# Kernel optimization log

Measured on AMD Instinct MI355X. Metric: run time of the kernel, lower is better.

## Reference

```python
import jax, jax.numpy as jnp
import numpy as np


def setup_inputs() -> dict:
    key = jax.random.key(0)
    ks = jax.random.split(key, 8)
    B, C, W, H = 4, 256, 64, 64
    Cq = C // 8
    return {
        "input": jax.random.normal(ks[0], (B, C, W, H), dtype=jnp.float32),
        "Wf": jax.random.normal(ks[1], (Cq, C), dtype=jnp.float32) * 0.05,
        "bf": jax.random.normal(ks[2], (Cq,), dtype=jnp.float32) * 0.05,
        "Wg": jax.random.normal(ks[3], (Cq, C), dtype=jnp.float32) * 0.05,
        "bg": jax.random.normal(ks[4], (Cq,), dtype=jnp.float32) * 0.05,
        "Wh": jax.random.normal(ks[5], (C, C), dtype=jnp.float32) * 0.05,
        "bh": jax.random.normal(ks[6], (C,), dtype=jnp.float32) * 0.05,
        "gamma": jax.random.normal(ks[7], (1,), dtype=jnp.float32),
    }


def reference(input, Wf, bf, Wg, bg, Wh, bh, gamma):
    # input: [B, C, W, H]; SAGAN self-attention over N = W*H spatial tokens.
    B, C, W, H = input.shape
    N = W * H
    x = input.reshape(B, C, N)
    # 1x1 Conv1d == per-token linear projection over channels.
    f = jnp.einsum('oc,bcn->bon', Wf, x) + bf[None, :, None]  # [B, C/8, N]
    g = jnp.einsum('oc,bcn->bon', Wg, x) + bg[None, :, None]  # [B, C/8, N]
    h = jnp.einsum('oc,bcn->bon', Wh, x) + bh[None, :, None]  # [B, C,   N]
    # s = f^T g -> [B, N, N]; softmax over last dim (columns / g-tokens).
    s = jnp.einsum('bon,bom->bnm', f, g)
    attention = jax.nn.softmax(s, axis=-1)
    # out = h @ attention^T : out[b,c,m] = sum_n h[b,c,n] * attention[b,m,n]
    out = jnp.einsum('bcn,bmn->bcm', h, attention)
    out = out.reshape(B, C, W, H)
    return gamma[0] * out + input
```

## Files before the change

### kernel.cpp

```cpp
#include <hip/hip_runtime.h>

typedef _Float16 half8 __attribute__((ext_vector_type(8)));
typedef _Float16 half4 __attribute__((ext_vector_type(4)));
typedef __fp16 f16x2 __attribute__((ext_vector_type(2)));
typedef __fp16 f16x4 __attribute__((ext_vector_type(4)));
typedef float floatx16 __attribute__((ext_vector_type(16)));

#define MFMA_F16(A, B, C) __builtin_amdgcn_mfma_f32_32x32x16_f16(A, B, C, 0, 0, 0)

constexpr int Bn = 4;
constexpr int Cc = 256;
constexpr int Cq = 32;
constexpr int Nn = 4096;
constexpr float LOG2E = 1.44269504088896340736f;


__device__ inline floatx16 zero16() {
  floatx16 z;
#pragma unroll
  for (int i = 0; i < 16; ++i) z[i] = 0.f;
  return z;
}

__global__ __launch_bounds__(256) void k_wconv(
    const float* __restrict__ Wf, const float* __restrict__ Wg,
    const float* __restrict__ Wh, _Float16* __restrict__ Wfh,
    _Float16* __restrict__ Wgh, _Float16* __restrict__ Whh) {
  int e = (blockIdx.x * 256 + threadIdx.x) * 4;
  const float* src;
  _Float16* dst;
  float sc = 1.f;
  if (e < 8192) { src = Wf + e; dst = Wfh + e; sc = LOG2E; }
  else if (e < 16384) { src = Wg + (e - 8192); dst = Wgh + (e - 8192); }
  else { src = Wh + (e - 16384); dst = Whh + (e - 16384); }
  float4 v = *(const float4*)src;
  half4 o;
  o[0] = (_Float16)(v.x * sc); o[1] = (_Float16)(v.y * sc);
  o[2] = (_Float16)(v.z * sc); o[3] = (_Float16)(v.w * sc);
  *(half4*)dst = o;
}

__global__ __launch_bounds__(256) void k_proj(
    const float* __restrict__ x,
    const _Float16* __restrict__ Wfh, const float* __restrict__ bf,
    const _Float16* __restrict__ Wgh, const float* __restrict__ bg,
    const _Float16* __restrict__ Whh, const float* __restrict__ bh,
    _Float16* __restrict__ Q, _Float16* __restrict__ K4,
    _Float16* __restrict__ V8) {
  __shared__ float xs[32][260];
  int tid = threadIdx.x;
  int w = tid >> 6, lane = tid & 63;
  int ml = lane & 31, h = lane >> 5;
  int b = blockIdx.x >> 7, nt = blockIdx.x & 127;
  int n0 = nt * 32;

  {
    int c = tid >> 3;
    int nl = (tid & 7) * 4;
    const float* xp = x + (size_t)b * Cc * Nn + n0 + nl;
#pragma unroll
    for (int pass = 0; pass < 8; ++pass) {
      int cc = c + pass * 32;
      float4 v = *(const float4*)(xp + (size_t)cc * Nn);
      xs[nl + 0][cc] = v.x;
      xs[nl + 1][cc] = v.y;
      xs[nl + 2][cc] = v.z;
      xs[nl + 3][cc] = v.w;
    }
  }
  __syncthreads();

  half8 bfr[16];
#pragma unroll
  for (int kc = 0; kc < 16; ++kc) {
    const float* xp = &xs[ml][kc * 16 + h * 8];
    half8 f;
#pragma unroll
    for (int j = 0; j < 8; ++j) f[j] = (_Float16)xp[j];
    bfr[kc] = f;
  }

  for (int t = w; t < 10; t += 4) {
    const _Float16* W;
    const float* bias;
    float bscale = 1.f;
    int o0 = 0;
    if (t == 0) { W = Wfh; bias = bf; bscale = LOG2E; }
    else if (t == 1) { W = Wgh; bias = bg; }
    else { W = Whh + (size_t)(t - 2) * 32 * Cc; bias = bh + (t - 2) * 32; o0 = (t - 2) * 32; }

    floatx16 acc = zero16();
    const _Float16* wp = W + (size_t)ml * Cc + h * 8;
#pragma unroll
    for (int kc = 0; kc < 16; ++kc) {
      half8 a = *(const half8*)(wp + kc * 16);
      acc = MFMA_F16(a, bfr[kc], acc);
    }

    if (t == 0) {
      _Float16* op = Q + ((size_t)b * Nn + n0 + ml) * Cq;
#pragma unroll
      for (int qd = 0; qd < 4; ++qd) {
        float4 bq = *(const float4*)(bias + 8 * qd + 4 * h);
        const float* bqp = (const float*)&bq;
#pragma unroll
        for (int i = 0; i < 4; ++i) {
          int crow = i + 8 * qd + 4 * h;
          op[crow] = (_Float16)(acc[4 * qd + i] + bqp[i] * bscale);
        }
      }
    } else if (t == 1) {
#pragma unroll
      for (int qd = 0; qd < 4; ++qd) {
        float4 bq = *(const float4*)(bias + 8 * qd + 4 * h);
        const float* bqp = (const float*)&bq;
#pragma unroll
        for (int i = 0; i < 4; ++i) {
          int crow = i + 8 * qd + 4 * h;
          K4[(((size_t)b * 4 + (crow >> 3)) * Nn + n0 + ml) * 8 + (crow & 7)] =
              (_Float16)(acc[4 * qd + i] + bqp[i]);
        }
      }
    } else {
      size_t nb = (size_t)((n0 + ml) >> 3);
      _Float16* op = V8 + (((size_t)b * 512 + nb) * 256) * 8 + (ml & 7);
#pragma unroll
      for (int qd = 0; qd < 4; ++qd) {
        float4 bq = *(const float4*)(bias + 8 * qd + 4 * h);
        const float* bqp = (const float*)&bq;
#pragma unroll
        for (int i = 0; i < 4; ++i) {
          int crow = i + 8 * qd + 4 * h;
          op[(size_t)(o0 + crow) * 8] = (_Float16)(acc[4 * qd + i] + bqp[i]);
        }
      }
    }
  }
}

__global__ __launch_bounds__(512) void k_rowmax(const _Float16* __restrict__ Q,
                                                const _Float16* __restrict__ K4,
                                                float* __restrict__ M) {
  __shared__ float red[8][32];
  int tid = threadIdx.x, w = tid >> 6, lane = tid & 63;
  int ml = lane & 31, h = lane >> 5;
  int b = blockIdx.x >> 7, mt = blockIdx.x & 127;
  int m0 = mt * 32;
  const _Float16* qp = Q + ((size_t)b * Nn + m0 + ml) * Cq + h * 8;
  half8 qb0 = *(const half8*)(qp);
  half8 qb1 = *(const half8*)(qp + 16);
  const _Float16* kp0 = K4 + (((size_t)b * 4 + h) * Nn + w * 512 + ml) * 8;
  const _Float16* kp1 = K4 + (((size_t)b * 4 + 2 + h) * Nn + w * 512 + ml) * 8;
  float mx = -3.0e38f;
  for (int t = 0; t < 16; ++t) {
    floatx16 s = zero16();
    half8 k0 = *(const half8*)(kp0 + (size_t)t * 32 * 8);
    half8 k1 = *(const half8*)(kp1 + (size_t)t * 32 * 8);
    s = MFMA_F16(k0, qb0, s);
    s = MFMA_F16(k1, qb1, s);
#pragma unroll
    for (int i = 0; i < 16; ++i) mx = fmaxf(mx, s[i]);
  }
  mx = fmaxf(mx, __shfl_xor(mx, 32, 64));
  if (h == 0) red[w][ml] = mx;
  __syncthreads();
  if (tid < 32) {
    float m2 = red[0][tid];
#pragma unroll
    for (int i = 1; i < 8; ++i) m2 = fmaxf(m2, red[i][tid]);
    M[(size_t)b * Nn + m0 + tid] = m2;
  }
}

__global__ __launch_bounds__(512, 4) void k_attn(
    const _Float16* __restrict__ Q, const _Float16* __restrict__ K4,
    const _Float16* __restrict__ V8, const float* __restrict__ M,
    _Float16* __restrict__ Opart, float* __restrict__ lpart, int nspan) {
  __shared__ _Float16 P[2 * 64 * 128];
  __shared__ float lred[8][32];
  int tid = threadIdx.x, w = tid >> 6, lane = tid & 63;
  int ml = lane & 31, h = lane >> 5;
  int msub = w & 1, nq = w >> 1;
  int bx = blockIdx.x;
  int mt = bx & 63, b = (bx >> 6) & 3, nc = bx >> 8;
  int m0 = mt * 64;
  int nbase0 = nc * nspan;
  int sw = ml & 15;

  const _Float16* qp = Q + ((size_t)b * Nn + m0 + msub * 32 + ml) * Cq + h * 8;
  half8 qb0 = *(const half8*)(qp);
  half8 qb1 = *(const half8*)(qp + 16);
  float Mv = M[(size_t)b * Nn + m0 + msub * 32 + ml];
  float lacc = 0.f;

  const _Float16* k4b0 =
      K4 + (((size_t)b * 4 + h) * Nn + nbase0 + nq * 32 + ml) * 8;
  const _Float16* k4b1 =
      K4 + (((size_t)b * 4 + 2 + h) * Nn + nbase0 + nq * 32 + ml) * 8;

  int c0 = w * 32;
  const _Float16* v8b =
      V8 + (((size_t)b * 512 + (nbase0 >> 3)) * 256 + c0 + ml) * 8;

  floatx16 o0 = zero16(), o1 = zero16();
  int iters = nspan >> 7;
  _Float16* pwbase = &P[(msub * 32 + ml) * 128];
  const _Float16* pr0 = &P[ml * 128];
  const _Float16* pr1 = &P[(32 + ml) * 128];

  for (int it = 0; it < iters; ++it) {
    int bufo = (it & 1) * (64 * 128);
    {
      floatx16 s = zero16();
      half8 k0 = *(const half8*)(k4b0 + (size_t)it * 128 * 8);
      half8 k1 = *(const half8*)(k4b1 + (size_t)it * 128 * 8);
      s = MFMA_F16(k0, qb0, s);
      s = MFMA_F16(k1, qb1, s);
      _Float16* pw = pwbase + bufo;
#pragma unroll
      for (int q = 0; q < 4; ++q) {
        float p0 = __builtin_amdgcn_exp2f(s[4 * q + 0] - Mv);
        float p1 = __builtin_amdgcn_exp2f(s[4 * q + 1] - Mv);
        float p2 = __builtin_amdgcn_exp2f(s[4 * q + 2] - Mv);
        float p3 = __builtin_amdgcn_exp2f(s[4 * q + 3] - Mv);
        lacc += (p0 + p1) + (p2 + p3);
        f16x4 pkv = __builtin_shufflevector(__builtin_amdgcn_cvt_pkrtz(p0, p1),
                                            __builtin_amdgcn_cvt_pkrtz(p2, p3),
                                            0, 1, 2, 3);
        half4 pk = __builtin_bit_cast(half4, pkv);
        *(half4*)(pw + ((nq * 4 + q) ^ sw) * 8 + 4 * h) = pk;
      }
    }
    __syncthreads();
    {
      const _Float16* vp = v8b + (size_t)it * 16 * 2048;
      const _Float16* p0b = pr0 + bufo;
      const _Float16* p1b = pr1 + bufo;
#pragma unroll
      for (int kc = 0; kc < 8; ++kc) {
        half8 vf = *(const half8*)(vp + (size_t)(kc * 2 + h) * 2048);
        int chunk = (kc * 2 + h) ^ sw;
        half8 pb0 = *(const half8*)(p0b + chunk * 8);
        half8 pb1 = *(const half8*)(p1b + chunk * 8);
        o0 = MFMA_F16(vf, pb0, o0);
        o1 = MFMA_F16(vf, pb1, o1);
      }
    }
  }

  lacc += __shfl_xor(lacc, 32, 64);
  if (h == 0) lred[w][ml] = lacc;
  __syncthreads();
  if (w < 2 && h == 0) {
    float lsum = lred[w][ml] + lred[w + 2][ml] + lred[w + 4][ml] + lred[w + 6][ml];
    lpart[((size_t)nc * Bn + b) * Nn + m0 + w * 32 + ml] = lsum;
  }

  _Float16* op0 = Opart + ((size_t)((size_t)nc * Bn + b) * Cc) * Nn + (m0 + ml);
#pragma unroll
  for (int r = 0; r < 16; ++r) {
    int c = c0 + (r & 3) + 8 * (r >> 2) + 4 * h;
    op0[(size_t)c * Nn] = (_Float16)o0[r];
    op0[(size_t)c * Nn + 32] = (_Float16)o1[r];
  }
}

__global__ __launch_bounds__(256) void k_fin(const _Float16* __restrict__ Op,
                                             const float* __restrict__ lp,
                                             const float* __restrict__ inp,
                                             const float* __restrict__ gamma,
                                             float* __restrict__ out, int NC) {
  int i4 = (blockIdx.x * 256 + threadIdx.x) * 4;
  int m = i4 & (Nn - 1);
  int bc = i4 >> 12;
  int b = bc >> 8;
  float ax = 0.f, ay = 0.f, az = 0.f, aw = 0.f;
  float lx = 0.f, ly = 0.f, lz = 0.f, lw = 0.f;
  for (int nc = 0; nc < NC; ++nc) {
    half4 o = *(const half4*)(Op + ((size_t)nc * Bn * Cc + bc) * Nn + m);
    float4 lv = *(const float4*)(lp + ((size_t)nc * Bn + b) * Nn + m);
    ax += (float)o[0]; ay += (float)o[1]; az += (float)o[2]; aw += (float)o[3];
    lx += lv.x; ly += lv.y; lz += lv.z; lw += lv.w;
  }
  float g = gamma[0];
  float4 xi = *(const float4*)(inp + (size_t)i4);
  float4 r;
  r.x = g * ax / lx + xi.x;
  r.y = g * ay / ly + xi.y;
  r.z = g * az / lz + xi.z;
  r.w = g * aw / lw + xi.w;
  *(float4*)(out + (size_t)i4) = r;
}

extern "C" void kernel_launch(void* const* d_in, const int* in_sizes, int n_in,
                              void* d_out, int out_size, void* d_ws,
                              size_t ws_size, hipStream_t stream) {
  const float* x = (const float*)d_in[0];
  const float* Wf = (const float*)d_in[1];
  const float* bf = (const float*)d_in[2];
  const float* Wg = (const float*)d_in[3];
  const float* bg = (const float*)d_in[4];
  const float* Wh = (const float*)d_in[5];
  const float* bh = (const float*)d_in[6];
  const float* gamma = (const float*)d_in[7];
  float* out = (float*)d_out;

  char* ws = (char*)d_ws;
  _Float16* Q  = (_Float16*)(ws);
  _Float16* K4 = (_Float16*)(ws + 1048576);
  _Float16* V8 = (_Float16*)(ws + 2097152);
  float*    M  = (float*)   (ws + 10485760);
  _Float16* Wfh = (_Float16*)(ws + 10551296);
  _Float16* Wgh = (_Float16*)(ws + 10567680);
  _Float16* Whh = (_Float16*)(ws + 10584064);

  size_t base = 10715136u;
  size_t per_chunk = 65536u + 8388608u;
  int NC = (ws_size >= base + 2u * per_chunk) ? 2 : 1;
  int nspan = Nn / NC;

  float*    lpart = (float*)(ws + base);
  _Float16* Opart = (_Float16*)(ws + base + (size_t)NC * 65536u);

  k_wconv<<<dim3(80), dim3(256), 0, stream>>>(Wf, Wg, Wh, Wfh, Wgh, Whh);
  k_proj<<<dim3(512), dim3(256), 0, stream>>>(x, Wfh, bf, Wgh, bg, Whh, bh, Q, K4, V8);
  k_rowmax<<<dim3(512), dim3(512), 0, stream>>>(Q, K4, M);
  k_attn<<<dim3(NC * 256), dim3(512), 0, stream>>>(Q, K4, V8, M, Opart, lpart, nspan);
  k_fin<<<dim3(4096), dim3(256), 0, stream>>>(Opart, lpart, x, gamma, out, NC);
}
```

Before: 165.4 us.

## Fuse attention finalize into k_attn with register-resident P and LDS tree reduction

The attention kernel is restructured so each block owns 32 query columns for all 256 channels. Each of its 8 waves handles a disjoint slice of keys. The softmax probabilities are rearranged into MFMA operand layout in registers with permlane32_swap instead of going through shared memory and a barrier. Partial outputs are reduced across waves with a shared-memory tree, then normalized, scaled by gamma and added to the residual in the same kernel. This removes the fp16 partial-output buffer, the separate k_fin launch and the per-iteration syncthreads. In exchange it needs 128 KB of LDS per block, a large register footprint, and several barriers in the reduction tail.

```diff
diff --git a/kernel.cpp b/kernel.cpp
--- a/kernel.cpp
+++ b/kernel.cpp
@@ -2,8 +2,8 @@
 
 typedef _Float16 half8 __attribute__((ext_vector_type(8)));
 typedef _Float16 half4 __attribute__((ext_vector_type(4)));
-typedef __fp16 f16x2 __attribute__((ext_vector_type(2)));
-typedef __fp16 f16x4 __attribute__((ext_vector_type(4)));
+typedef unsigned int uintx2 __attribute__((ext_vector_type(2)));
+typedef unsigned int uintx4 __attribute__((ext_vector_type(4)));
 typedef float floatx16 __attribute__((ext_vector_type(16)));
 
 #define MFMA_F16(A, B, C) __builtin_amdgcn_mfma_f32_32x32x16_f16(A, B, C, 0, 0, 0)
@@ -20,6 +20,10 @@
 #pragma unroll
   for (int i = 0; i < 16; ++i) z[i] = 0.f;
   return z;
+}
+
+__device__ inline unsigned int pkrtz(float a, float b) {
+  return __builtin_bit_cast(unsigned int, __builtin_amdgcn_cvt_pkrtz(a, b));
 }
 
 __global__ __launch_bounds__(256) void k_wconv(
@@ -172,124 +176,125 @@
   }
 }
 
-__global__ __launch_bounds__(512, 4) void k_attn(
+__device__ inline void otree_write(float2* dst, const floatx16* o) {
+#pragma unroll
+  for (int cb = 0; cb < 8; ++cb)
+#pragma unroll
+    for (int rp = 0; rp < 8; ++rp)
+      dst[(cb * 8 + rp) * 64] = make_float2(o[cb][2 * rp], o[cb][2 * rp + 1]);
+}
+
+__device__ inline void otree_add(const float2* src, floatx16* o) {
+#pragma unroll
+  for (int cb = 0; cb < 8; ++cb)
+#pragma unroll
+    for (int rp = 0; rp < 8; ++rp) {
+      float2 v = src[(cb * 8 + rp) * 64];
+      o[cb][2 * rp] += v.x;
+      o[cb][2 * rp + 1] += v.y;
+    }
+}
+
+__global__ __launch_bounds__(512, 2) void k_attn(
     const _Float16* __restrict__ Q, const _Float16* __restrict__ K4,
     const _Float16* __restrict__ V8, const float* __restrict__ M,
-    _Float16* __restrict__ Opart, float* __restrict__ lpart, int nspan) {
-  __shared__ _Float16 P[2 * 64 * 128];
+    const float* __restrict__ xin, const float* __restrict__ gamma,
+    float* __restrict__ out) {
+  __shared__ float Ored[4 * 8192];
   __shared__ float lred[8][32];
   int tid = threadIdx.x, w = tid >> 6, lane = tid & 63;
   int ml = lane & 31, h = lane >> 5;
-  int msub = w & 1, nq = w >> 1;
   int bx = blockIdx.x;
-  int mt = bx & 63, b = (bx >> 6) & 3, nc = bx >> 8;
-  int m0 = mt * 64;
-  int nbase0 = nc * nspan;
-  int sw = ml & 15;
-
-  const _Float16* qp = Q + ((size_t)b * Nn + m0 + msub * 32 + ml) * Cq + h * 8;
+  int mt = bx & 127, b = bx >> 7;
+  int m0 = mt * 32;
+
+  const _Float16* qp = Q + ((size_t)b * Nn + m0 + ml) * Cq + h * 8;
   half8 qb0 = *(const half8*)(qp);
   half8 qb1 = *(const half8*)(qp + 16);
-  float Mv = M[(size_t)b * Nn + m0 + msub * 32 + ml];
+  float Mv = M[(size_t)b * Nn + m0 + ml];
+  float g = gamma[0];
   float lacc = 0.f;
 
-  const _Float16* k4b0 =
-      K4 + (((size_t)b * 4 + h) * Nn + nbase0 + nq * 32 + ml) * 8;
-  const _Float16* k4b1 =
-      K4 + (((size_t)b * 4 + 2 + h) * Nn + nbase0 + nq * 32 + ml) * 8;
-
-  int c0 = w * 32;
-  const _Float16* v8b =
-      V8 + (((size_t)b * 512 + (nbase0 >> 3)) * 256 + c0 + ml) * 8;
-
-  floatx16 o0 = zero16(), o1 = zero16();
-  int iters = nspan >> 7;
-  _Float16* pwbase = &P[(msub * 32 + ml) * 128];
-  const _Float16* pr0 = &P[ml * 128];
-  const _Float16* pr1 = &P[(32 + ml) * 128];
-
-  for (int it = 0; it < iters; ++it) {
-    int bufo = (it & 1) * (64 * 128);
-    {
-      floatx16 s = zero16();
-      half8 k0 = *(const half8*)(k4b0 + (size_t)it * 128 * 8);
-      half8 k1 = *(const half8*)(k4b1 + (size_t)it * 128 * 8);
-      s = MFMA_F16(k0, qb0, s);
-      s = MFMA_F16(k1, qb1, s);
-      _Float16* pw = pwbase + bufo;
-#pragma unroll
-      for (int q = 0; q < 4; ++q) {
-        float p0 = __builtin_amdgcn_exp2f(s[4 * q + 0] - Mv);
-        float p1 = __builtin_amdgcn_exp2f(s[4 * q + 1] - Mv);
-        float p2 = __builtin_amdgcn_exp2f(s[4 * q + 2] - Mv);
-        float p3 = __builtin_amdgcn_exp2f(s[4 * q + 3] - Mv);
-        lacc += (p0 + p1) + (p2 + p3);
-        f16x4 pkv = __builtin_shufflevector(__builtin_amdgcn_cvt_pkrtz(p0, p1),
-                                            __builtin_amdgcn_cvt_pkrtz(p2, p3),
-                                            0, 1, 2, 3);
-        half4 pk = __builtin_bit_cast(half4, pkv);
-        *(half4*)(pw + ((nq * 4 + q) ^ sw) * 8 + 4 * h) = pk;
-      }
-    }
-    __syncthreads();
-    {
-      const _Float16* vp = v8b + (size_t)it * 16 * 2048;
-      const _Float16* p0b = pr0 + bufo;
-      const _Float16* p1b = pr1 + bufo;
-#pragma unroll
-      for (int kc = 0; kc < 8; ++kc) {
-        half8 vf = *(const half8*)(vp + (size_t)(kc * 2 + h) * 2048);
-        int chunk = (kc * 2 + h) ^ sw;
-        half8 pb0 = *(const half8*)(p0b + chunk * 8);
-        half8 pb1 = *(const half8*)(p1b + chunk * 8);
-        o0 = MFMA_F16(vf, pb0, o0);
-        o1 = MFMA_F16(vf, pb1, o1);
-      }
+  const _Float16* k4b0 = K4 + (((size_t)b * 4 + h) * Nn + w * 32 + ml) * 8;
+  const _Float16* k4b1 = K4 + (((size_t)b * 4 + 2 + h) * Nn + w * 32 + ml) * 8;
+  const _Float16* v8b = V8 + (((size_t)b * 512 + w * 4 + h) * 256 + ml) * 8;
+
+  floatx16 o[8];
+#pragma unroll
+  for (int i = 0; i < 8; ++i) o[i] = zero16();
+
+  half8 k0 = *(const half8*)(k4b0);
+  half8 k1 = *(const half8*)(k4b1);
+
+  for (int it = 0; it < 16; ++it) {
+    floatx16 s = zero16();
+    s = MFMA_F16(k0, qb0, s);
+    s = MFMA_F16(k1, qb1, s);
+    k0 = *(const half8*)(k4b0 + (size_t)(it + 1) * 2048);
+    k1 = *(const half8*)(k4b1 + (size_t)(it + 1) * 2048);
+    float p[16];
+#pragma unroll
+    for (int i = 0; i < 16; ++i) p[i] = __builtin_amdgcn_exp2f(s[i] - Mv);
+#pragma unroll
+    for (int i = 0; i < 16; ++i) lacc += p[i];
+    unsigned int c0 = pkrtz(p[0], p[1]),  c1 = pkrtz(p[2], p[3]);
+    unsigned int c2 = pkrtz(p[4], p[5]),  c3 = pkrtz(p[6], p[7]);
+    unsigned int c4 = pkrtz(p[8], p[9]),  c5 = pkrtz(p[10], p[11]);
+    unsigned int c6 = pkrtz(p[12], p[13]), c7 = pkrtz(p[14], p[15]);
+    uintx2 t02 = __builtin_amdgcn_permlane32_swap(c0, c2, false, false);
+    uintx2 t13 = __builtin_amdgcn_permlane32_swap(c1, c3, false, false);
+    uintx2 t46 = __builtin_amdgcn_permlane32_swap(c4, c6, false, false);
+    uintx2 t57 = __builtin_amdgcn_permlane32_swap(c5, c7, false, false);
+    uintx4 f0v = {t02.x, t13.x, t02.y, t13.y};
+    uintx4 f1v = {t46.x, t57.x, t46.y, t57.y};
+    half8 pf0 = __builtin_bit_cast(half8, f0v);
+    half8 pf1 = __builtin_bit_cast(half8, f1v);
+    const _Float16* vp = v8b + (size_t)it * 65536;
+#pragma unroll
+    for (int cb = 0; cb < 8; ++cb) {
+      half8 vf0 = *(const half8*)(vp + cb * 256);
+      o[cb] = MFMA_F16(vf0, pf0, o[cb]);
+    }
+#pragma unroll
+    for (int cb = 0; cb < 8; ++cb) {
+      half8 vf1 = *(const half8*)(vp + 4096 + cb * 256);
+      o[cb] = MFMA_F16(vf1, pf1, o[cb]);
     }
   }
 
   lacc += __shfl_xor(lacc, 32, 64);
   if (h == 0) lred[w][ml] = lacc;
-  __syncthreads();
-  if (w < 2 && h == 0) {
-    float lsum = lred[w][ml] + lred[w + 2][ml] + lred[w + 4][ml] + lred[w + 6][ml];
-    lpart[((size_t)nc * Bn + b) * Nn + m0 + w * 32 + ml] = lsum;
-  }
-
-  _Float16* op0 = Opart + ((size_t)((size_t)nc * Bn + b) * Cc) * Nn + (m0 + ml);
-#pragma unroll
-  for (int r = 0; r < 16; ++r) {
-    int c = c0 + (r & 3) + 8 * (r >> 2) + 4 * h;
-    op0[(size_t)c * Nn] = (_Float16)o0[r];
-    op0[(size_t)c * Nn + 32] = (_Float16)o1[r];
-  }
-}
-
-__global__ __launch_bounds__(256) void k_fin(const _Float16* __restrict__ Op,
-                                             const float* __restrict__ lp,
-                                             const float* __restrict__ inp,
-                                             const float* __restrict__ gamma,
-                                             float* __restrict__ out, int NC) {
-  int i4 = (blockIdx.x * 256 + threadIdx.x) * 4;
-  int m = i4 & (Nn - 1);
-  int bc = i4 >> 12;
-  int b = bc >> 8;
-  float ax = 0.f, ay = 0.f, az = 0.f, aw = 0.f;
-  float lx = 0.f, ly = 0.f, lz = 0.f, lw = 0.f;
-  for (int nc = 0; nc < NC; ++nc) {
-    half4 o = *(const half4*)(Op + ((size_t)nc * Bn * Cc + bc) * Nn + m);
-    float4 lv = *(const float4*)(lp + ((size_t)nc * Bn + b) * Nn + m);
-    ax += (float)o[0]; ay += (float)o[1]; az += (float)o[2]; aw += (float)o[3];
-    lx += lv.x; ly += lv.y; lz += lv.z; lw += lv.w;
-  }
-  float g = gamma[0];
-  float4 xi = *(const float4*)(inp + (size_t)i4);
-  float4 r;
-  r.x = g * ax / lx + xi.x;
-  r.y = g * ay / ly + xi.y;
-  r.z = g * az / lz + xi.z;
-  r.w = g * aw / lw + xi.w;
-  *(float4*)(out + (size_t)i4) = r;
+
+  float2* Ored2 = (float2*)Ored;
+  int lofs = h * 32 + ml;
+  if (w >= 4) otree_write(Ored2 + (w - 4) * 4096 + lofs, o);
+  __syncthreads();
+  if (w < 4) otree_add(Ored2 + w * 4096 + lofs, o);
+  __syncthreads();
+  if (w == 2 || w == 3) otree_write(Ored2 + (w - 2) * 4096 + lofs, o);
+  __syncthreads();
+  if (w < 2) otree_add(Ored2 + w * 4096 + lofs, o);
+  __syncthreads();
+  if (w == 1) otree_write(Ored2 + lofs, o);
+  __syncthreads();
+  if (w == 0) { otree_add(Ored2 + lofs, o); otree_write(Ored2 + lofs, o); }
+  __syncthreads();
+
+  float lv = 0.f;
+#pragma unroll
+  for (int i = 0; i < 8; ++i) lv += lred[i][ml];
+  float scale = g / lv;
+  const float2* src = Ored2 + lofs;
+  size_t obase = ((size_t)b * 256 + w * 32) * (size_t)Nn + m0 + ml;
+#pragma unroll
+  for (int rp = 0; rp < 8; ++rp) {
+    float2 v = src[(w * 8 + rp) * 64];
+    int r = 2 * rp;
+    int cA = (r & 3) + 8 * (r >> 2) + 4 * h;
+    size_t oa = obase + (size_t)cA * Nn;
+    out[oa] = scale * v.x + xin[oa];
+    out[oa + Nn] = scale * v.y + xin[oa + Nn];
+  }
 }
 
 extern "C" void kernel_launch(void* const* d_in, const int* in_sizes, int n_in,
@@ -314,17 +319,8 @@
   _Float16* Wgh = (_Float16*)(ws + 10567680);
   _Float16* Whh = (_Float16*)(ws + 10584064);
 
-  size_t base = 10715136u;
-  size_t per_chunk = 65536u + 8388608u;
-  int NC = (ws_size >= base + 2u * per_chunk) ? 2 : 1;
-  int nspan = Nn / NC;
-
-  float*    lpart = (float*)(ws + base);
-  _Float16* Opart = (_Float16*)(ws + base + (size_t)NC * 65536u);
-
   k_wconv<<<dim3(80), dim3(256), 0, stream>>>(Wf, Wg, Wh, Wfh, Wgh, Whh);
   k_proj<<<dim3(512), dim3(256), 0, stream>>>(x, Wfh, bf, Wgh, bg, Whh, bh, Q, K4, V8);
   k_rowmax<<<dim3(512), dim3(512), 0, stream>>>(Q, K4, M);
-  k_attn<<<dim3(NC * 256), dim3(512), 0, stream>>>(Q, K4, V8, M, Opart, lpart, nspan);
-  k_fin<<<dim3(4096), dim3(256), 0, stream>>>(Opart, lpart, x, gamma, out, NC);
-}
+  k_attn<<<dim3(512), dim3(512), 0, stream>>>(Q, K4, V8, M, x, gamma, out);
+}
```

Result: no change. 163.5 us (-1.2%).
